# Performance work log

Hardware: AMD Instinct MI355X
Metric: run time of the kernel (lower is better)

The kernel has to match this reference:

```python
import jax, jax.numpy as jnp
import numpy as np
import math

B, S, D, H = 4, 2048, 1024, 16
HD = D // H

def setup_inputs() -> dict:
    key = jax.random.key(0)
    k = jax.random.split(key, 5)
    scale = 1.0 / math.sqrt(D)
    return {
        "x": jax.random.normal(k[0], (B, S, D), dtype=jnp.float32),
        "W_qkv": jax.random.normal(k[1], (D, 3 * D), dtype=jnp.float32) * scale,
        "b_qkv": jnp.zeros((3 * D,), dtype=jnp.float32),
        "W_out": jax.random.normal(k[2], (D, D), dtype=jnp.float32) * scale,
        "b_out": jnp.zeros((D,), dtype=jnp.float32),
    }

def reference(x, W_qkv, b_qkv, W_out, b_out):
    b, s, d = x.shape
    qkv = x @ W_qkv + b_qkv                       # [b, s, 3d]
    qkv = qkv.reshape(b, s, 3, H, HD)
    q, k, v = jnp.moveaxis(qkv, 2, 0)             # each [b, s, H, HD]
    q = jnp.transpose(q, (0, 2, 1, 3))            # [b, H, s, hd]
    k = jnp.transpose(k, (0, 2, 1, 3))
    v = jnp.transpose(v, (0, 2, 1, 3))
    scores = jnp.einsum('bhqd,bhkd->bhqk', q, k) / math.sqrt(HD)
    causal = jnp.tril(jnp.ones((s, s), dtype=bool))
    scores = jnp.where(causal, scores, -jnp.inf)
    weights = jax.nn.softmax(scores, axis=-1)     # dropout = identity (eval)
    attended = jnp.einsum('bhqk,bhkd->bhqd', weights, v)
    attended = jnp.transpose(attended, (0, 2, 1, 3)).reshape(b, s, d)
    return attended @ W_out + b_out
```

## Files before the change

kernel.cpp:

```cpp
#include <hip/hip_runtime.h>
#include <hip/hip_bf16.h>

typedef __attribute__((ext_vector_type(4))) float f32x4;
typedef __attribute__((ext_vector_type(16))) float f32x16;
typedef __attribute__((ext_vector_type(8))) short short8;

static constexpr int Ssz = 2048;
static constexpr int Dsz = 1024;

__device__ __forceinline__ unsigned short f2bf(float f){
  union { float f; unsigned u; } c; c.f = f;
  unsigned r = c.u + 0x7fffu + ((c.u >> 16) & 1u);
  return (unsigned short)(r >> 16);
}

__device__ __forceinline__ void gl2lds16(const void* g, void* l){
  __builtin_amdgcn_global_load_lds(
    (const __attribute__((address_space(1))) unsigned int*)g,
    (__attribute__((address_space(3))) unsigned int*)l, 16, 0, 0);
}

__device__ __forceinline__ unsigned cvtpk(float lo, float hi){
  unsigned r;
  asm("v_cvt_pk_bf16_f32 %0, %1, %2" : "=v"(r) : "v"(lo), "v"(hi));
  return r;
}

__device__ __forceinline__ void permswap(unsigned &a, unsigned &b){
  asm volatile("v_permlane32_swap_b32 %0, %1" : "+v"(a), "+v"(b));
}

__device__ __forceinline__ float xmax64(float x){
  float a = x, b;
  asm volatile("v_mov_b32 %0, %1" : "=v"(b) : "v"(a));
  asm volatile("v_permlane32_swap_b32 %0, %1" : "+v"(a), "+v"(b));
  return fmaxf(a, b);
}
__device__ __forceinline__ float xsum64(float x){
  float a = x, b;
  asm volatile("v_mov_b32 %0, %1" : "=v"(b) : "v"(a));
  asm volatile("v_permlane32_swap_b32 %0, %1" : "+v"(a), "+v"(b));
  return a + b;
}

__global__ void cvt_kernel(const float* __restrict__ in, unsigned short* __restrict__ out, int n){
  int i = (blockIdx.x * 256 + threadIdx.x) * 8;
  if (i >= n) return;
  float4 a = *(const float4*)(in + i);
  float4 b = *(const float4*)(in + i + 4);
  short8 o;
  o[0]=(short)f2bf(a.x); o[1]=(short)f2bf(a.y); o[2]=(short)f2bf(a.z); o[3]=(short)f2bf(a.w);
  o[4]=(short)f2bf(b.x); o[5]=(short)f2bf(b.y); o[6]=(short)f2bf(b.z); o[7]=(short)f2bf(b.w);
  *(short8*)(out + i) = o;
}

__global__ void transpose_kernel(const float* __restrict__ in, unsigned short* __restrict__ out,
                                 int R, int C){
  __shared__ float tile[32][33];
  int c0 = blockIdx.x * 32, r0 = blockIdx.y * 32;
  int tx = threadIdx.x, ty = threadIdx.y;
  #pragma unroll
  for (int k = 0; k < 4; ++k)
    tile[ty + 8*k][tx] = in[(size_t)(r0 + ty + 8*k) * C + c0 + tx];
  __syncthreads();
  #pragma unroll
  for (int k = 0; k < 4; ++k)
    out[(size_t)(c0 + ty + 8*k) * R + r0 + tx] = f2bf(tile[tx][ty + 8*k]);
}

#define BM 128
#define BN 128
#define BKg 64

__global__ __launch_bounds__(256, 2)
void gemm_bt(const unsigned short* __restrict__ A, const unsigned short* __restrict__ Bt,
             int M, int N, int K,
             const float* __restrict__ bias, int mode,
             unsigned short* __restrict__ Qp, unsigned short* __restrict__ Kp,
             unsigned short* __restrict__ Vtp, float* __restrict__ Out)
{
  __shared__ unsigned short ldsA[BM * BKg];
  __shared__ unsigned short ldsB[BN * BKg];
  const int tid = threadIdx.x;
  const int wid = tid >> 6;
  const int lane = tid & 63;
  const int lr = lane & 15, lg = lane >> 4;
  const int wr = wid >> 1, wc = wid & 1;
  const int m0 = blockIdx.y * BM, n0 = blockIdx.x * BN;

  const f32x4 vzero = {0.f, 0.f, 0.f, 0.f};
  f32x4 acc[4][4];
  #pragma unroll
  for (int i = 0; i < 4; ++i)
    #pragma unroll
    for (int j = 0; j < 4; ++j) acc[i][j] = vzero;

  for (int k0 = 0; k0 < K; k0 += BKg){
    __syncthreads();
    #pragma unroll
    for (int it = 0; it < 4; ++it){
      int c = it * 256 + tid;
      int row = c >> 3;
      int sc = (c & 7) ^ (row & 7);
      gl2lds16(A  + (size_t)(m0 + row) * K + k0 + sc * 8,
               (char*)ldsA + (it * 256 + wid * 64) * 16);
      gl2lds16(Bt + (size_t)(n0 + row) * K + k0 + sc * 8,
               (char*)ldsB + (it * 256 + wid * 64) * 16);
    }
    __syncthreads();
    #pragma unroll
    for (int kc = 0; kc < 2; ++kc){
      short8 af[4], bfr[4];
      #pragma unroll
      for (int i = 0; i < 4; ++i){
        int row = wr * 64 + i * 16 + lr;
        int off = row * 128 + lg * 16 + kc * 64;
        off ^= (row & 7) << 4;
        af[i] = *(const short8*)((const char*)ldsA + off);
      }
      #pragma unroll
      for (int j = 0; j < 4; ++j){
        int row = wc * 64 + j * 16 + lr;
        int off = row * 128 + lg * 16 + kc * 64;
        off ^= (row & 7) << 4;
        bfr[j] = *(const short8*)((const char*)ldsB + off);
      }
      #pragma unroll
      for (int i = 0; i < 4; ++i)
        #pragma unroll
        for (int j = 0; j < 4; ++j)
          acc[i][j] = __builtin_amdgcn_mfma_f32_16x16x32_bf16(af[i], bfr[j], acc[i][j], 0, 0, 0);
    }
  }

  if (mode == 0){
    const float qscale = 0.125f * 1.4426950408889634f;
    #pragma unroll
    for (int i = 0; i < 4; ++i)
      #pragma unroll
      for (int j = 0; j < 4; ++j)
        #pragma unroll
        for (int r = 0; r < 4; ++r){
          int gm = m0 + wr * 64 + i * 16 + lg * 4 + r;
          int gn = n0 + wc * 64 + j * 16 + lr;
          float v = acc[i][j][r] + bias[gn];
          int which = gn >> 10;
          int h = (gn >> 6) & 15;
          int hd = gn & 63;
          int b = gm >> 11;
          int s = gm & 2047;
          size_t bh = (size_t)(b * 16 + h);
          if (which == 0)      Qp[(bh * Ssz + s) * 64 + hd] = f2bf(v * qscale);
          else if (which == 1) Kp[(bh * Ssz + s) * 64 + hd] = f2bf(v);
          else                 Vtp[(bh * 64 + hd) * Ssz + s] = f2bf(v);
        }
  } else {
    #pragma unroll
    for (int i = 0; i < 4; ++i)
      #pragma unroll
      for (int j = 0; j < 4; ++j)
        #pragma unroll
        for (int r = 0; r < 4; ++r){
          int gm = m0 + wr * 64 + i * 16 + lg * 4 + r;
          int gn = n0 + wc * 64 + j * 16 + lr;
          Out[(size_t)gm * N + gn] = acc[i][j][r] + bias[gn];
        }
  }
}

__global__ __launch_bounds__(256, 2)
void attn_kernel(const unsigned short* __restrict__ Qp, const unsigned short* __restrict__ Kp,
                 const unsigned short* __restrict__ Vtp, unsigned short* __restrict__ Att)
{
  __shared__ unsigned short ldsK[2][4096];
  __shared__ unsigned short ldsV[2][4096];
  const int tid = threadIdx.x;
  const int wid = tid >> 6;
  const int lane = tid & 63;
  const int lq = lane & 31;
  const int hi = lane >> 5;

  const int flat = (int)blockIdx.x + 8 * (int)blockIdx.y;
  const int xcd = flat & 7;
  const int i6  = flat >> 3;
  const int bh  = xcd * 8 + (i6 >> 3);
  const int qx  = i6 & 7;
  const int b = bh >> 4, hh = bh & 15;

  #pragma unroll 1
  for (int job = 0; job < 2; ++job){
    const int qt = job ? (15 - qx) : qx;
    const int q0w = qt * 128 + wid * 32;
    const int qa = q0w + lq;
    const int nt = 2 * qt + 2;

    short8 qf[4];
    {
      const unsigned short* Qb = Qp + ((size_t)bh * Ssz + q0w + lq) * 64 + hi * 8;
      #pragma unroll
      for (int ks = 0; ks < 4; ++ks) qf[ks] = *(const short8*)(Qb + ks * 16);
    }

    f32x16 Ot[2];
    #pragma unroll
    for (int d = 0; d < 2; ++d)
      #pragma unroll
      for (int r = 0; r < 16; ++r) Ot[d][r] = 0.f;
    float mrun = -3e38f, lsum = 0.f;

    #pragma unroll
    for (int it = 0; it < 2; ++it){
      int c = it * 256 + tid;
      int row = c >> 3, sc = (c & 7) ^ (row & 7);
      gl2lds16(Kp  + ((size_t)bh * Ssz + row) * 64 + sc * 8,
               (char*)&ldsK[0][0] + (it * 256 + wid * 64) * 16);
      gl2lds16(Vtp + ((size_t)bh * 64 + row) * Ssz + sc * 8,
               (char*)&ldsV[0][0] + (it * 256 + wid * 64) * 16);
    }
    __syncthreads();

    for (int kt = 0; kt < nt; ++kt){
      const int cur = kt & 1;
      if (kt + 1 < nt){
        const int nxt = cur ^ 1;
        #pragma unroll
        for (int it = 0; it < 2; ++it){
          int c = it * 256 + tid;
          int row = c >> 3, sc = (c & 7) ^ (row & 7);
          gl2lds16(Kp  + ((size_t)bh * Ssz + (kt + 1) * 64 + row) * 64 + sc * 8,
                   (char*)&ldsK[nxt][0] + (it * 256 + wid * 64) * 16);
          gl2lds16(Vtp + ((size_t)bh * 64 + row) * Ssz + (kt + 1) * 64 + sc * 8,
                   (char*)&ldsV[nxt][0] + (it * 256 + wid * 64) * 16);
        }
      }

      if (kt * 64 <= q0w + 31){
        const char* Kb = (const char*)&ldsK[cur][0];
        const char* Vb = (const char*)&ldsV[cur][0];

        f32x16 S[2];
        #pragma unroll
        for (int kb = 0; kb < 2; ++kb)
          #pragma unroll
          for (int r = 0; r < 16; ++r) S[kb][r] = 0.f;
        #pragma unroll
        for (int ks = 0; ks < 4; ++ks){
          int col = 32 * ks + 16 * hi;
          int r0 = lq, r1 = 32 + lq;
          short8 k0 = *(const short8*)(Kb + ((r0 * 128 + col) ^ ((r0 & 7) << 4)));
          short8 k1 = *(const short8*)(Kb + ((r1 * 128 + col) ^ ((r1 & 7) << 4)));
          S[0] = __builtin_amdgcn_mfma_f32_32x32x16_bf16(k0, qf[ks], S[0], 0, 0, 0);
          S[1] = __builtin_amdgcn_mfma_f32_32x32x16_bf16(k1, qf[ks], S[1], 0, 0, 0);
        }

        if (kt * 64 + 63 > q0w){
          #pragma unroll
          for (int r = 0; r < 16; ++r){
            int keyb = kt * 64 + (r & 3) + ((r >> 2) << 3) + 4 * hi;
            if (keyb > qa)      S[0][r] = -3e38f;
            if (keyb + 32 > qa) S[1][r] = -3e38f;
          }
        }

        float t16[16];
        #pragma unroll
        for (int r = 0; r < 16; ++r) t16[r] = fmaxf(S[0][r], S[1][r]);
        float t8[8];
        #pragma unroll
        for (int r = 0; r < 8; ++r) t8[r] = fmaxf(t16[r], t16[r + 8]);
        float t4[4];
        #pragma unroll
        for (int r = 0; r < 4; ++r) t4[r] = fmaxf(t8[r], t8[r + 4]);
        float pmax = fmaxf(fmaxf(t4[0], t4[1]), fmaxf(t4[2], t4[3]));
        pmax = xmax64(pmax);

        if (!__all(pmax - mrun <= 8.0f)){
          float mn = fmaxf(mrun, pmax);
          float scl = __builtin_amdgcn_exp2f(mrun - mn);
          mrun = mn;
          lsum *= scl;
          #pragma unroll
          for (int d = 0; d < 2; ++d)
            #pragma unroll
            for (int r = 0; r < 16; ++r) Ot[d][r] *= scl;
        }

        #pragma unroll
        for (int kb = 0; kb < 2; ++kb)
          #pragma unroll
          for (int r = 0; r < 16; ++r)
            S[kb][r] = __builtin_amdgcn_exp2f(S[kb][r] - mrun);

        #pragma unroll
        for (int r = 0; r < 16; ++r) t16[r] = S[0][r] + S[1][r];
        #pragma unroll
        for (int r = 0; r < 8; ++r) t8[r] = t16[r] + t16[r + 8];
        #pragma unroll
        for (int r = 0; r < 4; ++r) t4[r] = t8[r] + t8[r + 4];
        float psum = (t4[0] + t4[1]) + (t4[2] + t4[3]);
        psum = xsum64(psum);
        lsum += psum;

        #pragma unroll
        for (int s = 0; s < 4; ++s){
          const int sb = s >> 1, s1 = s & 1;
          unsigned u0 = cvtpk(S[sb][8 * s1 + 0], S[sb][8 * s1 + 1]);
          unsigned u1 = cvtpk(S[sb][8 * s1 + 2], S[sb][8 * s1 + 3]);
          unsigned u2 = cvtpk(S[sb][8 * s1 + 4], S[sb][8 * s1 + 5]);
          unsigned u3 = cvtpk(S[sb][8 * s1 + 6], S[sb][8 * s1 + 7]);
          permswap(u0, u2);
          permswap(u1, u3);
          union { unsigned u[4]; short8 s8; } pb;
          pb.u[0] = u0; pb.u[1] = u1; pb.u[2] = u2; pb.u[3] = u3;

          int col = 32 * s + 16 * hi;
          int r0 = lq, r1 = 32 + lq;
          short8 v0 = *(const short8*)(Vb + ((r0 * 128 + col) ^ ((r0 & 7) << 4)));
          short8 v1 = *(const short8*)(Vb + ((r1 * 128 + col) ^ ((r1 & 7) << 4)));
          Ot[0] = __builtin_amdgcn_mfma_f32_32x32x16_bf16(v0, pb.s8, Ot[0], 0, 0, 0);
          Ot[1] = __builtin_amdgcn_mfma_f32_32x32x16_bf16(v1, pb.s8, Ot[1], 0, 0, 0);
        }
      }
      __syncthreads();
    }

    float inv = 1.0f / lsum;
    unsigned short* ep = &ldsK[0][0] + wid * 2048;
    #pragma unroll
    for (int d = 0; d < 2; ++d)
      #pragma unroll
      for (int g = 0; g < 4; ++g)
        #pragma unroll
        for (int cp = 0; cp < 2; ++cp){
          int r = g * 4 + cp * 2;
          unsigned w = cvtpk(Ot[d][r] * inv, Ot[d][r + 1] * inv);
          int dd = d * 32 + g * 8 + 4 * hi + cp * 2;
          int byte = lq * 128 + ((dd * 2) ^ ((lq & 7) << 4));
          *(unsigned*)((char*)ep + byte) = w;
        }
    __syncthreads();
    #pragma unroll
    for (int ii = 0; ii < 4; ++ii){
      int qr = ii * 8 + (lane >> 3);
      int cc = lane & 7;
      int byte = qr * 128 + ((cc * 16) ^ ((qr & 7) << 4));
      short8 vv = *(const short8*)((const char*)ep + byte);
      *(short8*)(Att + ((size_t)(b * Ssz + q0w + qr)) * Dsz + hh * 64 + cc * 8) = vv;
    }
    __syncthreads();
  }
}

extern "C" void kernel_launch(void* const* d_in, const int* in_sizes, int n_in,
                              void* d_out, int out_size, void* d_ws, size_t ws_size,
                              hipStream_t stream) {
  const float* x    = (const float*)d_in[0];
  const float* Wqkv = (const float*)d_in[1];
  const float* bqkv = (const float*)d_in[2];
  const float* Wout = (const float*)d_in[3];
  const float* bout = (const float*)d_in[4];
  float* out = (float*)d_out;

  unsigned short* xb    = (unsigned short*)d_ws;
  unsigned short* wqkvT = xb    + (size_t)8192 * 1024;
  unsigned short* woutT = wqkvT + (size_t)3072 * 1024;
  unsigned short* Qb    = woutT + (size_t)1024 * 1024;
  unsigned short* Kb    = Qb    + (size_t)8388608;
  unsigned short* Vtb   = Kb    + (size_t)8388608;
  unsigned short* Attb  = Vtb   + (size_t)8388608;

  cvt_kernel<<<4096, 256, 0, stream>>>(x, xb, 8388608);
  transpose_kernel<<<dim3(96, 32), dim3(32, 8), 0, stream>>>(Wqkv, wqkvT, 1024, 3072);
  transpose_kernel<<<dim3(32, 32), dim3(32, 8), 0, stream>>>(Wout, woutT, 1024, 1024);
  gemm_bt<<<dim3(24, 64), 256, 0, stream>>>(xb, wqkvT, 8192, 3072, 1024,
                                            bqkv, 0, Qb, Kb, Vtb, nullptr);
  attn_kernel<<<dim3(8, 64), 256, 0, stream>>>(Qb, Kb, Vtb, Attb);
  gemm_bt<<<dim3(8, 64), 256, 0, stream>>>(Attb, woutT, 8192, 1024, 1024,
                                           bout, 1, nullptr, nullptr, nullptr, out);
}
```

Baseline: 178.7 us.

## Load K/V attention fragments directly from global into registers, drop LDS staging

The attention kernel no longer stages K and V tiles through double-buffered LDS with block-wide barriers. Each wave now loads its MFMA operand fragments straight from global memory into registers, software-pipelined two tiles at a time. LDS is used only for the per-wave output transpose, with a waitcnt replacing the barriers. This removes the per-tile barriers and LDS traffic. In exchange, every wave separately re-reads the same K/V data from global memory or cache, and the extra fragment buffers raise register pressure.

```diff
diff --git a/kernel.cpp b/kernel.cpp
--- a/kernel.cpp
+++ b/kernel.cpp
@@ -172,8 +172,7 @@
 void attn_kernel(const unsigned short* __restrict__ Qp, const unsigned short* __restrict__ Kp,
                  const unsigned short* __restrict__ Vtp, unsigned short* __restrict__ Att)
 {
-  __shared__ unsigned short ldsK[2][4096];
-  __shared__ unsigned short ldsV[2][4096];
+  __shared__ unsigned short ldsE[4][2048];
   const int tid = threadIdx.x;
   const int wid = tid >> 6;
   const int lane = tid & 63;
@@ -187,6 +186,11 @@
   const int qx  = i6 & 7;
   const int b = bh >> 4, hh = bh & 15;
 
+  const unsigned short* kr0 = Kp  + (size_t)bh * Ssz * 64 + (size_t)lq * 64 + hi * 8;
+  const unsigned short* kr1 = kr0 + 32 * 64;
+  const unsigned short* vr0 = Vtp + (size_t)bh * 64 * Ssz + (size_t)lq * Ssz + hi * 8;
+  const unsigned short* vr1 = vr0 + (size_t)32 * Ssz;
+
   #pragma unroll 1
   for (int job = 0; job < 2; ++job){
     const int qt = job ? (15 - qx) : qx;
@@ -208,124 +212,123 @@
       for (int r = 0; r < 16; ++r) Ot[d][r] = 0.f;
     float mrun = -3e38f, lsum = 0.f;
 
-    #pragma unroll
-    for (int it = 0; it < 2; ++it){
-      int c = it * 256 + tid;
-      int row = c >> 3, sc = (c & 7) ^ (row & 7);
-      gl2lds16(Kp  + ((size_t)bh * Ssz + row) * 64 + sc * 8,
-               (char*)&ldsK[0][0] + (it * 256 + wid * 64) * 16);
-      gl2lds16(Vtp + ((size_t)bh * 64 + row) * Ssz + sc * 8,
-               (char*)&ldsV[0][0] + (it * 256 + wid * 64) * 16);
-    }
-    __syncthreads();
-
-    for (int kt = 0; kt < nt; ++kt){
-      const int cur = kt & 1;
-      if (kt + 1 < nt){
-        const int nxt = cur ^ 1;
-        #pragma unroll
-        for (int it = 0; it < 2; ++it){
-          int c = it * 256 + tid;
-          int row = c >> 3, sc = (c & 7) ^ (row & 7);
-          gl2lds16(Kp  + ((size_t)bh * Ssz + (kt + 1) * 64 + row) * 64 + sc * 8,
-                   (char*)&ldsK[nxt][0] + (it * 256 + wid * 64) * 16);
-          gl2lds16(Vtp + ((size_t)bh * 64 + row) * Ssz + (kt + 1) * 64 + sc * 8,
-                   (char*)&ldsV[nxt][0] + (it * 256 + wid * 64) * 16);
-        }
-      }
-
-      if (kt * 64 <= q0w + 31){
-        const char* Kb = (const char*)&ldsK[cur][0];
-        const char* Vb = (const char*)&ldsV[cur][0];
-
-        f32x16 S[2];
-        #pragma unroll
-        for (int kb = 0; kb < 2; ++kb)
+    auto TILE = [&](int kt, const short8* kf, const short8* vf){
+      if (kt * 64 > q0w + 31) return;
+
+      f32x16 S[2];
+      #pragma unroll
+      for (int kb2 = 0; kb2 < 2; ++kb2)
+        #pragma unroll
+        for (int r = 0; r < 16; ++r) S[kb2][r] = 0.f;
+      #pragma unroll
+      for (int ks = 0; ks < 4; ++ks){
+        S[0] = __builtin_amdgcn_mfma_f32_32x32x16_bf16(kf[2*ks],   qf[ks], S[0], 0, 0, 0);
+        S[1] = __builtin_amdgcn_mfma_f32_32x32x16_bf16(kf[2*ks+1], qf[ks], S[1], 0, 0, 0);
+      }
+
+      if (kt * 64 + 63 > q0w){
+        #pragma unroll
+        for (int r = 0; r < 16; ++r){
+          int keyb = kt * 64 + (r & 3) + ((r >> 2) << 3) + 4 * hi;
+          if (keyb > qa)      S[0][r] = -3e38f;
+          if (keyb + 32 > qa) S[1][r] = -3e38f;
+        }
+      }
+
+      float t16[16];
+      #pragma unroll
+      for (int r = 0; r < 16; ++r) t16[r] = fmaxf(S[0][r], S[1][r]);
+      float t8[8];
+      #pragma unroll
+      for (int r = 0; r < 8; ++r) t8[r] = fmaxf(t16[r], t16[r + 8]);
+      float t4[4];
+      #pragma unroll
+      for (int r = 0; r < 4; ++r) t4[r] = fmaxf(t8[r], t8[r + 4]);
+      float pmax = fmaxf(fmaxf(t4[0], t4[1]), fmaxf(t4[2], t4[3]));
+      pmax = xmax64(pmax);
+
+      if (!__all(pmax - mrun <= 8.0f)){
+        float mn = fmaxf(mrun, pmax);
+        float scl = __builtin_amdgcn_exp2f(mrun - mn);
+        mrun = mn;
+        lsum *= scl;
+        #pragma unroll
+        for (int d = 0; d < 2; ++d)
           #pragma unroll
-          for (int r = 0; r < 16; ++r) S[kb][r] = 0.f;
+          for (int r = 0; r < 16; ++r) Ot[d][r] *= scl;
+      }
+
+      #pragma unroll
+      for (int kb2 = 0; kb2 < 2; ++kb2)
+        #pragma unroll
+        for (int r = 0; r < 16; ++r)
+          S[kb2][r] = __builtin_amdgcn_exp2f(S[kb2][r] - mrun);
+
+      #pragma unroll
+      for (int r = 0; r < 16; ++r) t16[r] = S[0][r] + S[1][r];
+      #pragma unroll
+      for (int r = 0; r < 8; ++r) t8[r] = t16[r] + t16[r + 8];
+      #pragma unroll
+      for (int r = 0; r < 4; ++r) t4[r] = t8[r] + t8[r + 4];
+      float psum = (t4[0] + t4[1]) + (t4[2] + t4[3]);
+      psum = xsum64(psum);
+      lsum += psum;
+
+      #pragma unroll
+      for (int s = 0; s < 4; ++s){
+        const int sb = s >> 1, s1 = s & 1;
+        unsigned u0 = cvtpk(S[sb][8 * s1 + 0], S[sb][8 * s1 + 1]);
+        unsigned u1 = cvtpk(S[sb][8 * s1 + 2], S[sb][8 * s1 + 3]);
+        unsigned u2 = cvtpk(S[sb][8 * s1 + 4], S[sb][8 * s1 + 5]);
+        unsigned u3 = cvtpk(S[sb][8 * s1 + 6], S[sb][8 * s1 + 7]);
+        permswap(u0, u2);
+        permswap(u1, u3);
+        union { unsigned u[4]; short8 s8; } pb;
+        pb.u[0] = u0; pb.u[1] = u1; pb.u[2] = u2; pb.u[3] = u3;
+        Ot[0] = __builtin_amdgcn_mfma_f32_32x32x16_bf16(vf[2*s],   pb.s8, Ot[0], 0, 0, 0);
+        Ot[1] = __builtin_amdgcn_mfma_f32_32x32x16_bf16(vf[2*s+1], pb.s8, Ot[1], 0, 0, 0);
+      }
+    };
+
+    short8 kfA[8], kfB[8], vfA[8], vfB[8];
+
+    #pragma unroll
+    for (int ks = 0; ks < 4; ++ks){
+      kfA[2*ks]   = *(const short8*)(kr0 + ks * 16);
+      kfA[2*ks+1] = *(const short8*)(kr1 + ks * 16);
+    }
+
+    #pragma unroll 1
+    for (int kt = 0; kt < nt; kt += 2){
+      #pragma unroll
+      for (int s = 0; s < 4; ++s){
+        vfA[2*s]   = *(const short8*)(vr0 + kt * 64 + s * 16);
+        vfA[2*s+1] = *(const short8*)(vr1 + kt * 64 + s * 16);
+      }
+      #pragma unroll
+      for (int ks = 0; ks < 4; ++ks){
+        kfB[2*ks]   = *(const short8*)(kr0 + (size_t)(kt + 1) * 4096 + ks * 16);
+        kfB[2*ks+1] = *(const short8*)(kr1 + (size_t)(kt + 1) * 4096 + ks * 16);
+      }
+      TILE(kt, kfA, vfA);
+
+      #pragma unroll
+      for (int s = 0; s < 4; ++s){
+        vfB[2*s]   = *(const short8*)(vr0 + (kt + 1) * 64 + s * 16);
+        vfB[2*s+1] = *(const short8*)(vr1 + (kt + 1) * 64 + s * 16);
+      }
+      if (kt + 2 < nt){
         #pragma unroll
         for (int ks = 0; ks < 4; ++ks){
-          int col = 32 * ks + 16 * hi;
-          int r0 = lq, r1 = 32 + lq;
-          short8 k0 = *(const short8*)(Kb + ((r0 * 128 + col) ^ ((r0 & 7) << 4)));
-          short8 k1 = *(const short8*)(Kb + ((r1 * 128 + col) ^ ((r1 & 7) << 4)));
-          S[0] = __builtin_amdgcn_mfma_f32_32x32x16_bf16(k0, qf[ks], S[0], 0, 0, 0);
-          S[1] = __builtin_amdgcn_mfma_f32_32x32x16_bf16(k1, qf[ks], S[1], 0, 0, 0);
-        }
-
-        if (kt * 64 + 63 > q0w){
-          #pragma unroll
-          for (int r = 0; r < 16; ++r){
-            int keyb = kt * 64 + (r & 3) + ((r >> 2) << 3) + 4 * hi;
-            if (keyb > qa)      S[0][r] = -3e38f;
-            if (keyb + 32 > qa) S[1][r] = -3e38f;
-          }
-        }
-
-        float t16[16];
-        #pragma unroll
-        for (int r = 0; r < 16; ++r) t16[r] = fmaxf(S[0][r], S[1][r]);
-        float t8[8];
-        #pragma unroll
-        for (int r = 0; r < 8; ++r) t8[r] = fmaxf(t16[r], t16[r + 8]);
-        float t4[4];
-        #pragma unroll
-        for (int r = 0; r < 4; ++r) t4[r] = fmaxf(t8[r], t8[r + 4]);
-        float pmax = fmaxf(fmaxf(t4[0], t4[1]), fmaxf(t4[2], t4[3]));
-        pmax = xmax64(pmax);
-
-        if (!__all(pmax - mrun <= 8.0f)){
-          float mn = fmaxf(mrun, pmax);
-          float scl = __builtin_amdgcn_exp2f(mrun - mn);
-          mrun = mn;
-          lsum *= scl;
-          #pragma unroll
-          for (int d = 0; d < 2; ++d)
-            #pragma unroll
-            for (int r = 0; r < 16; ++r) Ot[d][r] *= scl;
-        }
-
-        #pragma unroll
-        for (int kb = 0; kb < 2; ++kb)
-          #pragma unroll
-          for (int r = 0; r < 16; ++r)
-            S[kb][r] = __builtin_amdgcn_exp2f(S[kb][r] - mrun);
-
-        #pragma unroll
-        for (int r = 0; r < 16; ++r) t16[r] = S[0][r] + S[1][r];
-        #pragma unroll
-        for (int r = 0; r < 8; ++r) t8[r] = t16[r] + t16[r + 8];
-        #pragma unroll
-        for (int r = 0; r < 4; ++r) t4[r] = t8[r] + t8[r + 4];
-        float psum = (t4[0] + t4[1]) + (t4[2] + t4[3]);
-        psum = xsum64(psum);
-        lsum += psum;
-
-        #pragma unroll
-        for (int s = 0; s < 4; ++s){
-          const int sb = s >> 1, s1 = s & 1;
-          unsigned u0 = cvtpk(S[sb][8 * s1 + 0], S[sb][8 * s1 + 1]);
-          unsigned u1 = cvtpk(S[sb][8 * s1 + 2], S[sb][8 * s1 + 3]);
-          unsigned u2 = cvtpk(S[sb][8 * s1 + 4], S[sb][8 * s1 + 5]);
-          unsigned u3 = cvtpk(S[sb][8 * s1 + 6], S[sb][8 * s1 + 7]);
-          permswap(u0, u2);
-          permswap(u1, u3);
-          union { unsigned u[4]; short8 s8; } pb;
-          pb.u[0] = u0; pb.u[1] = u1; pb.u[2] = u2; pb.u[3] = u3;
-
-          int col = 32 * s + 16 * hi;
-          int r0 = lq, r1 = 32 + lq;
-          short8 v0 = *(const short8*)(Vb + ((r0 * 128 + col) ^ ((r0 & 7) << 4)));
-          short8 v1 = *(const short8*)(Vb + ((r1 * 128 + col) ^ ((r1 & 7) << 4)));
-          Ot[0] = __builtin_amdgcn_mfma_f32_32x32x16_bf16(v0, pb.s8, Ot[0], 0, 0, 0);
-          Ot[1] = __builtin_amdgcn_mfma_f32_32x32x16_bf16(v1, pb.s8, Ot[1], 0, 0, 0);
-        }
-      }
-      __syncthreads();
+          kfA[2*ks]   = *(const short8*)(kr0 + (size_t)(kt + 2) * 4096 + ks * 16);
+          kfA[2*ks+1] = *(const short8*)(kr1 + (size_t)(kt + 2) * 4096 + ks * 16);
+        }
+      }
+      TILE(kt + 1, kfB, vfB);
     }
 
     float inv = 1.0f / lsum;
-    unsigned short* ep = &ldsK[0][0] + wid * 2048;
+    unsigned short* ep = &ldsE[wid][0];
     #pragma unroll
     for (int d = 0; d < 2; ++d)
       #pragma unroll
@@ -338,7 +341,7 @@
           int byte = lq * 128 + ((dd * 2) ^ ((lq & 7) << 4));
           *(unsigned*)((char*)ep + byte) = w;
         }
-    __syncthreads();
+    asm volatile("s_waitcnt lgkmcnt(0)" ::: "memory");
     #pragma unroll
     for (int ii = 0; ii < 4; ++ii){
       int qr = ii * 8 + (lane >> 3);
@@ -347,7 +350,6 @@
       short8 vv = *(const short8*)((const char*)ep + byte);
       *(short8*)(Att + ((size_t)(b * Ssz + q0w + qr)) * Dsz + hh * 64 + cc * 8) = vv;
     }
-    __syncthreads();
   }
 }
 
```

Result: slower. 245.2 us (+37.2%).
